# Performance work log

Hardware: AMD Instinct MI355X
Metric: run time of the kernel (lower is better)

The kernel has to match this reference:

```python
import jax, jax.numpy as jnp
import numpy as np
import math

B, N, DIM, H, DH, NNULL = 2, 2048, 1024, 16, 64, 2
SCALE = 8.0
LN_EPS = 1e-5


def _alibi_slopes(heads):
    # heads is a power of 2 here (16): slopes = start * start**i
    start = 2.0 ** (-(2.0 ** (-(math.log2(heads) - 3))))
    return np.array([start * (start ** i) for i in range(heads)], dtype=np.float32)


def setup_inputs() -> dict:
    key = jax.random.key(0)
    ks = jax.random.split(key, 6)
    inner = H * DH
    return {
        "x": jax.random.normal(ks[0], (B, N, DIM), dtype=jnp.float32),
        "norm_g": jnp.ones((DIM,), jnp.float32),
        "norm_b": jnp.zeros((DIM,), jnp.float32),
        "Wq": jax.random.normal(ks[1], (DIM, inner), jnp.float32) * 0.02,
        "Wkv": jax.random.normal(ks[2], (DIM, 2 * inner), jnp.float32) * 0.02,
        "q_scale": jnp.ones((DH,), jnp.float32),
        "k_scale": jnp.ones((DH,), jnp.float32),
        "null_kv": jax.random.normal(ks[3], (H, 2 * NNULL, DH), jnp.float32),
        "Wout": jax.random.normal(ks[4], (inner, DIM), jnp.float32) * 0.02,
    }


def _l2norm(t):
    # matches F.normalize: x / max(||x||, 1e-12)
    n = jnp.sqrt(jnp.sum(t * t, axis=-1, keepdims=True))
    return t / jnp.maximum(n, 1e-12)


def reference(x, norm_g, norm_b, Wq, Wkv, q_scale, k_scale, null_kv, Wout):
    b, n, dim = x.shape
    h, dh, nn = H, DH, NNULL
    j = n + nn

    # NOTE: faithful to source -- K/V come from the PRE-norm x (kv_input bound
    # before x = self.norm(x)); only Q uses the LayerNorm'd x.
    mu = jnp.mean(x, axis=-1, keepdims=True)
    var = jnp.mean((x - mu) ** 2, axis=-1, keepdims=True)
    xn = (x - mu) * jax.lax.rsqrt(var + LN_EPS) * norm_g + norm_b

    q = (xn @ Wq).reshape(b, n, h, dh).transpose(0, 2, 1, 3)          # b h n d
    kv = x @ Wkv
    k, v = jnp.split(kv, 2, axis=-1)
    k = k.reshape(b, n, h, dh).transpose(0, 2, 1, 3)                   # b h n d
    v = v.reshape(b, n, h, dh).transpose(0, 2, 1, 3)

    # null kv: (h, 2*nn, dh) -> (h, nn, 2, dh)
    null = null_kv.reshape(h, nn, 2, dh)
    nk = jnp.broadcast_to(null[:, :, 0, :][None], (b, h, nn, dh))
    nv = jnp.broadcast_to(null[:, :, 1, :][None], (b, h, nn, dh))
    k = jnp.concatenate([nk, k], axis=2)                               # b h j d
    v = jnp.concatenate([nv, v], axis=2)

    q = _l2norm(q) * q_scale
    k = _l2norm(k) * k_scale

    sim = jnp.einsum('bhid,bhjd->bhij', q, k) * SCALE                  # b h n j

    # ALiBi bias: rows at positions j-n..j-1, cols 0..j-1
    irow = jnp.arange(j - n, j)
    jcol = jnp.arange(j)
    bias = -jnp.abs(jcol[None, :] - irow[:, None]).astype(sim.dtype)   # (n, j)
    slopes = jnp.asarray(_alibi_slopes(h))[:, None, None]              # (h,1,1)
    sim = sim + slopes * bias

    # causal mask: triu with offset j - n + 1 (null kv always visible)
    causal = jnp.triu(jnp.ones((n, j), dtype=bool), k=j - n + 1)
    neg = jnp.finfo(sim.dtype).max
    sim = jnp.where(causal[None, None], -neg, sim)

    attn = jax.nn.softmax(sim, axis=-1)
    out = jnp.einsum('bhij,bhjd->bhid', attn, v)
    out = out.transpose(0, 2, 1, 3).reshape(b, n, h * dh)
    return out @ Wout
```

## Files before the change

kernel.cpp:

```cpp
#include <hip/hip_runtime.h>
#include <hip/hip_bf16.h>
#include <stdint.h>

#define H_    16
#define N_    2048
#define DIM_  1024
#define DH_   64
#define NN_   2
#define J_    2050
#define JP_   2112
#define B_    2
#define M_    4096
#define NSEG_ 84

typedef unsigned short u16;
typedef unsigned int u32;
typedef short bf16x8 __attribute__((ext_vector_type(8)));
typedef float f32x4 __attribute__((ext_vector_type(4)));

__device__ __forceinline__ u16 f2b(float f) {
  union { float f; unsigned int i; } v; v.f = f;
  unsigned int r = v.i + 0x7fffu + ((v.i >> 16) & 1u);
  return (u16)(r >> 16);
}
__device__ __forceinline__ float b2f(u16 u) {
  union { unsigned int i; float f; } v; v.i = ((unsigned int)u) << 16; return v.f;
}
__device__ __forceinline__ float lo2f(u32 u) {
  union { u32 i; float f; } v; v.i = u << 16; return v.f;
}
__device__ __forceinline__ float hi2f(u32 u) {
  union { u32 i; float f; } v; v.i = u & 0xffff0000u; return v.f;
}
__device__ __forceinline__ void unp8(const uint4 u, float* d) {
  d[0] = lo2f(u.x); d[1] = hi2f(u.x); d[2] = lo2f(u.y); d[3] = hi2f(u.y);
  d[4] = lo2f(u.z); d[5] = hi2f(u.z); d[6] = lo2f(u.w); d[7] = hi2f(u.w);
}
__device__ __forceinline__ u32 pk2(float a, float b) {
  union { __hip_bfloat162 h; u32 u; } x;
  x.h = __float22bfloat162_rn(make_float2(a, b));
  return x.u;
}
__device__ __forceinline__ void dma16(const u16* g, u16* l) {
  __builtin_amdgcn_global_load_lds(
      (const __attribute__((address_space(1))) u32*)(const void*)g,
      (__attribute__((address_space(3))) u32*)(void*)l, 16, 0, 0);
}

__global__ __launch_bounds__(256) void ktranspose_cast(const float* __restrict__ in,
                                                       u16* __restrict__ out, int R, int C) {
  __shared__ float tile[32][33];
  int tx = threadIdx.x & 31, ty = threadIdx.x >> 5;
  int c0 = blockIdx.x * 32, r0 = blockIdx.y * 32;
  #pragma unroll
  for (int i = 0; i < 32; i += 8)
    tile[ty + i][tx] = in[(size_t)(r0 + ty + i) * C + c0 + tx];
  __syncthreads();
  #pragma unroll
  for (int i = 0; i < 32; i += 8)
    out[(size_t)(c0 + ty + i) * R + r0 + tx] = f2b(tile[tx][ty + i]);
}

__global__ __launch_bounds__(256) void lnorm_k(const float* __restrict__ x,
                                               const float* __restrict__ g,
                                               const float* __restrict__ bb,
                                               u16* __restrict__ xn,
                                               u16* __restrict__ xbf) {
  int row = blockIdx.x;
  int t = threadIdx.x;
  float4 rw = *(const float4*)(x + (size_t)row * DIM_ + t * 4);
  float v0 = rw.x, v1 = rw.y, v2 = rw.z, v3 = rw.w;
  uint2 cw;
  cw.x = pk2(v0, v1);
  cw.y = pk2(v2, v3);
  *(uint2*)(xbf + (size_t)row * DIM_ + t * 4) = cw;
  float s = v0 + v1 + v2 + v3;
  float ss = v0 * v0 + v1 * v1 + v2 * v2 + v3 * v3;
  #pragma unroll
  for (int o = 32; o; o >>= 1) { s += __shfl_xor(s, o, 64); ss += __shfl_xor(ss, o, 64); }
  __shared__ float red[8];
  int lane = t & 63, w = t >> 6;
  if (lane == 0) { red[w] = s; red[4 + w] = ss; }
  __syncthreads();
  float S = red[0] + red[1] + red[2] + red[3];
  float SS = red[4] + red[5] + red[6] + red[7];
  float mu = S * (1.0f / DIM_);
  float var = SS * (1.0f / DIM_) - mu * mu;
  float rs = rsqrtf(var + 1e-5f);
  float4 gv = *(const float4*)(g + t * 4);
  float4 bv = *(const float4*)(bb + t * 4);
  uint2 ow;
  ow.x = pk2((v0 - mu) * rs * gv.x + bv.x, (v1 - mu) * rs * gv.y + bv.y);
  ow.y = pk2((v2 - mu) * rs * gv.z + bv.z, (v3 - mu) * rs * gv.w + bv.w);
  *(uint2*)(xn + (size_t)row * DIM_ + t * 4) = ow;
}

template <int MODE>
__global__ __launch_bounds__(256) void gemm_k(const u16* __restrict__ A,
                                              const u16* __restrict__ BT,
                                              void* __restrict__ dst0,
                                              void* __restrict__ dst1,
                                              const float* __restrict__ scale,
                                              int M, int Nc, int K) {
  __shared__ u16 As[128 * 64];
  __shared__ u16 Bs[64 * 64];
  int tid = threadIdx.x, wv = tid >> 6, lane = tid & 63;
  int fm = lane & 15, fg = lane >> 4;
  int row0 = blockIdx.y * 128, col0 = blockIdx.x * 64;
  f32x4 acc[2][4] = {};
  int srow = lane >> 3;
  int skb = ((lane & 7) ^ srow) * 8;
  const u16* Ag = A + (size_t)(row0 + wv * 32 + srow) * K + skb;
  const u16* Bg = BT + (size_t)(col0 + wv * 16 + srow) * K + skb;
  u16* AsW = As + (wv * 32) * 64;
  u16* BsW = Bs + (wv * 16) * 64;
  int fr7 = fm & 7;
  int ak0 = (fg ^ fr7) * 8;
  int ak1 = ((fg + 4) ^ fr7) * 8;
  for (int k0 = 0; k0 < K; k0 += 64) {
    __syncthreads();
    dma16(Ag + k0,                    AsW);
    dma16(Ag + (size_t)8 * K + k0,    AsW + 8 * 64);
    dma16(Ag + (size_t)16 * K + k0,   AsW + 16 * 64);
    dma16(Ag + (size_t)24 * K + k0,   AsW + 24 * 64);
    dma16(Bg + k0,                    BsW);
    dma16(Bg + (size_t)8 * K + k0,    BsW + 8 * 64);
    __syncthreads();
    bf16x8 af0[2], af1[2], bf0[4], bf1[4];
    #pragma unroll
    for (int mt = 0; mt < 2; mt++) {
      int rbase = (wv * 32 + mt * 16 + fm) * 64;
      af0[mt] = *(const bf16x8*)&As[rbase + ak0];
      af1[mt] = *(const bf16x8*)&As[rbase + ak1];
    }
    #pragma unroll
    for (int nt = 0; nt < 4; nt++) {
      int rbase = (nt * 16 + fm) * 64;
      bf0[nt] = *(const bf16x8*)&Bs[rbase + ak0];
      bf1[nt] = *(const bf16x8*)&Bs[rbase + ak1];
    }
    #pragma unroll
    for (int mt = 0; mt < 2; mt++)
      #pragma unroll
      for (int nt = 0; nt < 4; nt++) {
        acc[mt][nt] = __builtin_amdgcn_mfma_f32_16x16x32_bf16(af0[mt], bf0[nt], acc[mt][nt], 0, 0, 0);
        acc[mt][nt] = __builtin_amdgcn_mfma_f32_16x16x32_bf16(af1[mt], bf1[nt], acc[mt][nt], 0, 0, 0);
      }
  }
  if (MODE == 1) {
    float* C = (float*)dst0;
    #pragma unroll
    for (int mt = 0; mt < 2; mt++)
      #pragma unroll
      for (int r = 0; r < 4; r++) {
        int m = row0 + wv * 32 + mt * 16 + fg * 4 + r;
        #pragma unroll
        for (int nt = 0; nt < 4; nt++)
          C[(size_t)m * Nc + col0 + nt * 16 + fm] = acc[mt][nt][r];
      }
  } else {
    bool isK = (MODE == 2) || (col0 < 1024);
    int h = (isK ? col0 : col0 - 1024) >> 6;
    float sv[4];
    if (isK) {
      #pragma unroll
      for (int nt = 0; nt < 4; nt++) sv[nt] = scale[nt * 16 + fm];
    }
    u16* Do = (u16*)((MODE == 3 && !isK) ? dst1 : dst0);
    #pragma unroll
    for (int mt = 0; mt < 2; mt++) {
      #pragma unroll
      for (int r = 0; r < 4; r++) {
        float inv = 1.0f;
        if (isK) {
          float ssp = 0.0f;
          #pragma unroll
          for (int nt = 0; nt < 4; nt++) ssp += acc[mt][nt][r] * acc[mt][nt][r];
          #pragma unroll
          for (int o = 1; o <= 8; o <<= 1) ssp += __shfl_xor(ssp, o, 64);
          inv = 1.0f / fmaxf(sqrtf(ssp), 1e-12f);
        }
        int m = row0 + wv * 32 + mt * 16 + fg * 4 + r;
        int b = m >> 11, n = m & 2047;
        size_t base;
        if (MODE == 2)      base = (((size_t)(b * H_ + h)) * N_ + n) * 64;
        else if (isK)       base = (((size_t)(b * H_ + h)) * JP_ + (n + NN_)) * 64;
        else                base = (((size_t)(b * H_ + h)) * J_ + (n + NN_)) * 64;
        #pragma unroll
        for (int nt = 0; nt < 4; nt++) {
          float val = acc[mt][nt][r];
          if (isK) val = val * inv * sv[nt];
          Do[base + nt * 16 + fm] = f2b(val);
        }
      }
    }
  }
}

__global__ __launch_bounds__(256) void vtransp_k(const u16* __restrict__ Vb,
                                                 const float* __restrict__ nkv,
                                                 const float* __restrict__ ks,
                                                 u16* __restrict__ Kb,
                                                 u16* __restrict__ VTp) {
  __shared__ u16 tile[64][80];
  int t = threadIdx.x;
  int c = blockIdx.x, bh = blockIdx.y, h = bh & 15;
  int jl = t >> 2, dc = (t & 3) * 16;
  int j = c * 64 + jl;
  if (j < NN_) {
    float kvv[16];
    float kssp = 0.0f;
    #pragma unroll
    for (int e = 0; e < 16; e++) {
      float vv = nkv[(size_t)(h * 4 + 2 * j + 1) * 64 + dc + e];
      tile[jl][dc + e] = f2b(vv);
      float kv = nkv[(size_t)(h * 4 + 2 * j) * 64 + dc + e];
      kvv[e] = kv; kssp += kv * kv;
    }
    kssp += __shfl_xor(kssp, 1, 64);
    kssp += __shfl_xor(kssp, 2, 64);
    float inv = 1.0f / fmaxf(sqrtf(kssp), 1e-12f);
    #pragma unroll
    for (int e = 0; e < 16; e++)
      Kb[((size_t)bh * JP_ + j) * 64 + dc + e] = f2b(kvv[e] * inv * ks[dc + e]);
  } else if (j < J_) {
    const uint4* src = (const uint4*)(Vb + ((size_t)bh * J_ + j) * 64 + dc);
    *(uint4*)&tile[jl][dc] = src[0];
    *(uint4*)&tile[jl][dc + 8] = src[1];
  } else {
    uint4 z = {0, 0, 0, 0};
    *(uint4*)&tile[jl][dc] = z;
    *(uint4*)&tile[jl][dc + 8] = z;
  }
  __syncthreads();
  int d = t >> 2, p0 = (t & 3) * 16;
  u16 tmp[16] __attribute__((aligned(16)));
  #pragma unroll
  for (int e = 0; e < 16; e++) {
    int pos = p0 + e;
    int h2 = pos >> 5, rem = pos & 31;
    int fgp = rem >> 3, tt = rem & 7;
    int nt = tt >> 2, r = tt & 3;
    int jloc = (h2 * 2 + nt) * 16 + fgp * 4 + r;
    tmp[e] = tile[jloc][d];
  }
  uint4* dstp = (uint4*)(VTp + ((size_t)bh * 64 + d) * JP_ + c * 64 + p0);
  dstp[0] = ((uint4*)tmp)[0];
  dstp[1] = ((uint4*)tmp)[1];
}

__global__ __launch_bounds__(256, 6) void attn_k(const u16* __restrict__ Qn,
                                                 const u16* __restrict__ Kb,
                                                 const u16* __restrict__ VTp,
                                                 const float* __restrict__ qs,
                                                 const float* __restrict__ ks,
                                                 u16* __restrict__ partials) {
  __shared__ u16 Ks0[64 * 32], Ks1[64 * 32];
  __shared__ u16 Vs0[64 * 32], Vs1[64 * 32];
  int tid = threadIdx.x;
  int wv = tid >> 6, lane = tid & 63;
  int fm = lane & 15, fg = lane >> 4;
  int bh = blockIdx.y, h = bh & 15;
  int cum = 0, qt = 0, seg = 0;
  #pragma unroll 1
  for (int i = 0; i < 32; i++) {
    int t = 31 - i, s = (t + 9) >> 3;
    if ((int)blockIdx.x < cum + s) { qt = t; seg = (int)blockIdx.x - cum; break; }
    cum += s;
  }
  int q0 = qt * 64;
  int q = q0 + wv * 16 + fm;
  float slope = exp2f(-0.5f * (float)(h + 1));
  float prod = fabsf(qs[lane] * ks[lane]);
  #pragma unroll
  for (int o = 32; o; o >>= 1) prod = fmaxf(prod, __shfl_xor(prod, o, 64));
  float Mb = 8.0f * prod;
  const u16* qp = Qn + ((size_t)bh * N_ + q) * 64 + fg * 8;
  bf16x8 qf0 = *(const bf16x8*)(qp);
  bf16x8 qf1 = *(const bf16x8*)(qp + 32);
  f32x4 accO[4] = {};
  float lp = 0.0f;
  int lr = lane >> 2;
  int kbs = ((lane & 3) ^ ((lane >> 3) & 3)) * 8;
  int fs = (fg ^ ((fm >> 1) & 3)) * 8;
  const u16* KbBH = Kb + (size_t)bh * JP_ * 64;
  const u16* VTbh = VTp + (size_t)bh * 64 * JP_;
  int c0 = seg * 8;
  int c1 = min(c0 + 8, qt + 2);
  for (int c = c0; c < c1; c++) {
    int jb = c * 64;
    __syncthreads();
    const u16* Kg = KbBH + (size_t)(jb + wv * 16 + lr) * 64 + kbs;
    dma16(Kg,      Ks0 + wv * 512);
    dma16(Kg + 32, Ks1 + wv * 512);
    const u16* Vg = VTbh + (size_t)(wv * 16 + lr) * JP_ + jb + kbs;
    dma16(Vg,      Vs0 + wv * 512);
    dma16(Vg + 32, Vs1 + wv * 512);
    __syncthreads();
    f32x4 accS[4] = {};
    #pragma unroll
    for (int nt = 0; nt < 4; nt++) {
      bf16x8 kf0 = *(const bf16x8*)&Ks0[(nt * 16 + fm) * 32 + fs];
      accS[nt] = __builtin_amdgcn_mfma_f32_16x16x32_bf16(kf0, qf0, accS[nt], 0, 0, 0);
      bf16x8 kf1 = *(const bf16x8*)&Ks1[(nt * 16 + fm) * 32 + fs];
      accS[nt] = __builtin_amdgcn_mfma_f32_16x16x32_bf16(kf1, qf1, accS[nt], 0, 0, 0);
    }
    union { bf16x8 v; u16 s[8]; } P0, P1;
    #pragma unroll
    for (int nt = 0; nt < 4; nt++) {
      #pragma unroll
      for (int r = 0; r < 4; r++) {
        int jj = jb + nt * 16 + fg * 4 + r;
        float arg = fmaf(accS[nt][r], 8.0f, slope * (float)(jj - q - 2)) - Mb;
        float p = (jj <= q + 2) ? __expf(arg) : 0.0f;
        u16 pb = f2b(p);
        lp += b2f(pb);
        if (nt < 2) P0.s[nt * 4 + r] = pb;
        else        P1.s[(nt - 2) * 4 + r] = pb;
      }
    }
    #pragma unroll
    for (int nt = 0; nt < 4; nt++) {
      bf16x8 vf0 = *(const bf16x8*)&Vs0[(nt * 16 + fm) * 32 + fs];
      accO[nt] = __builtin_amdgcn_mfma_f32_16x16x32_bf16(vf0, P0.v, accO[nt], 0, 0, 0);
      bf16x8 vf1 = *(const bf16x8*)&Vs1[(nt * 16 + fm) * 32 + fs];
      accO[nt] = __builtin_amdgcn_mfma_f32_16x16x32_bf16(vf1, P1.v, accO[nt], 0, 0, 0);
    }
  }
  lp += __shfl_xor(lp, 16, 64);
  lp += __shfl_xor(lp, 32, 64);
  u16* P = partials + ((size_t)bh * NSEG_ + blockIdx.x) * 4224;
  int sq = wv * 16 + fm;
  #pragma unroll
  for (int nt = 0; nt < 4; nt++) {
    uint2 ow;
    ow.x = pk2(accO[nt][0], accO[nt][1]);
    ow.y = pk2(accO[nt][2], accO[nt][3]);
    *(uint2*)(P + sq * 64 + nt * 16 + fg * 4) = ow;
  }
  if (fg == 0) *(float*)(P + 4096 + 2 * sq) = lp;
}

__global__ __launch_bounds__(256) void comb_k(const u16* __restrict__ partials,
                                              u16* __restrict__ AO) {
  int qt = blockIdx.x, bh = blockIdx.y, b = bh >> 4, h = bh & 15;
  int t = threadIdx.x, q = t >> 2, dq = (t & 3) * 16;
  int s = (qt + 9) >> 3;
  int cum = 0;
  for (int tt = qt + 1; tt < 32; tt++) cum += (tt + 9) >> 3;
  float acc[16] = {};
  float lsum = 0.0f;
  for (int k = 0; k < s; k++) {
    const u16* P = partials + ((size_t)bh * NSEG_ + cum + k) * 4224;
    uint4 a = *(const uint4*)(P + q * 64 + dq);
    uint4 bq = *(const uint4*)(P + q * 64 + dq + 8);
    float tmp[8];
    unp8(a, tmp);
    #pragma unroll
    for (int e = 0; e < 8; e++) acc[e] += tmp[e];
    unp8(bq, tmp);
    #pragma unroll
    for (int e = 0; e < 8; e++) acc[8 + e] += tmp[e];
    lsum += *(const float*)(P + 4096 + 2 * q);
  }
  float linv = 1.0f / lsum;
  int n = qt * 64 + q;
  u16* dst = AO + (((size_t)(b * N_ + n)) * H_ + h) * 64 + dq;
  u16 ov[16] __attribute__((aligned(16)));
  #pragma unroll
  for (int e = 0; e < 16; e++) ov[e] = f2b(acc[e] * linv);
  *(uint4*)dst = ((uint4*)ov)[0];
  *(uint4*)(dst + 8) = ((uint4*)ov)[1];
}

extern "C" void kernel_launch(void* const* d_in, const int* in_sizes, int n_in,
                              void* d_out, int out_size, void* d_ws, size_t ws_size,
                              hipStream_t stream) {
  const float* x    = (const float*)d_in[0];
  const float* ng   = (const float*)d_in[1];
  const float* nb   = (const float*)d_in[2];
  const float* Wq   = (const float*)d_in[3];
  const float* Wkv  = (const float*)d_in[4];
  const float* qs   = (const float*)d_in[5];
  const float* ks   = (const float*)d_in[6];
  const float* nkv  = (const float*)d_in[7];
  const float* Wout = (const float*)d_in[8];
  float* out = (float*)d_out;
  char* ws = (char*)d_ws;

  u16* xn    = (u16*)(ws + 0);
  u16* WoutT = (u16*)(ws + 8388608);
  u16* Qn    = (u16*)(ws + 10485760);
  u16* Kb    = (u16*)(ws + 18874368);
  u16* VTp   = (u16*)(ws + 27525120);
  u16* xbf   = (u16*)(ws + 36175872);
  u16* WqT   = (u16*)(ws + 44564480);
  u16* WkvT  = (u16*)(ws + 46661632);
  u16* Vb    = (u16*)(ws + 50855936);
  u16* parts = xbf;
  u16* AO    = xn;

  hipMemsetAsync(Kb, 0, 8650752, stream);
  ktranspose_cast<<<dim3(32, 32), 256, 0, stream>>>(Wq, WqT, 1024, 1024);
  ktranspose_cast<<<dim3(64, 32), 256, 0, stream>>>(Wkv, WkvT, 1024, 2048);
  ktranspose_cast<<<dim3(32, 32), 256, 0, stream>>>(Wout, WoutT, 1024, 1024);
  lnorm_k<<<4096, 256, 0, stream>>>(x, ng, nb, xn, xbf);
  gemm_k<2><<<dim3(16, 32), 256, 0, stream>>>(xn, WqT, Qn, nullptr, qs, M_, 1024, 1024);
  gemm_k<3><<<dim3(32, 32), 256, 0, stream>>>(xbf, WkvT, Kb, Vb, ks, M_, 2048, 1024);
  vtransp_k<<<dim3(33, 32), 256, 0, stream>>>(Vb, nkv, ks, Kb, VTp);
  attn_k<<<dim3(NSEG_, 32), 256, 0, stream>>>(Qn, Kb, VTp, qs, ks, parts);
  comb_k<<<dim3(32, 32), 256, 0, stream>>>(parts, AO);
  gemm_k<1><<<dim3(16, 32), 256, 0, stream>>>(AO, WoutT, out, nullptr, nullptr, M_, 1024, 1024);
}
```

Before: 231.3 us.

## Merge launches and load GEMM A-operand directly into registers with prefetch

Merges the three weight transposes into one launch and the Q and KV projections into one GEMM launch, which cuts launch count and tail effects. The full-buffer memset of K is dropped; only the padding rows are zeroed inside the V-transpose kernel. The GEMM core now loads A fragments straight from global memory into registers, prefetched one K-step ahead, instead of staging them in LDS. This removes LDS traffic and part of the sync cost, but A reads are no longer shared through LDS across waves, and each lane issues strided global loads.

```diff
diff --git a/kernel.cpp b/kernel.cpp
--- a/kernel.cpp
+++ b/kernel.cpp
@@ -47,11 +47,21 @@
       (__attribute__((address_space(3))) u32*)(void*)l, 16, 0, 0);
 }
 
-__global__ __launch_bounds__(256) void ktranspose_cast(const float* __restrict__ in,
-                                                       u16* __restrict__ out, int R, int C) {
+__global__ __launch_bounds__(256) void wtrans_k(const float* __restrict__ Wq,
+                                                const float* __restrict__ Wkv,
+                                                const float* __restrict__ Wout,
+                                                u16* __restrict__ WqT,
+                                                u16* __restrict__ WkvT,
+                                                u16* __restrict__ WoutT) {
   __shared__ float tile[32][33];
+  int bx = blockIdx.x;
+  const float* in; u16* out; int C, cx;
+  if (bx < 32)      { in = Wq;   out = WqT;   C = 1024; cx = bx; }
+  else if (bx < 96) { in = Wkv;  out = WkvT;  C = 2048; cx = bx - 32; }
+  else              { in = Wout; out = WoutT; C = 1024; cx = bx - 96; }
+  const int R = 1024;
   int tx = threadIdx.x & 31, ty = threadIdx.x >> 5;
-  int c0 = blockIdx.x * 32, r0 = blockIdx.y * 32;
+  int c0 = cx * 32, r0 = blockIdx.y * 32;
   #pragma unroll
   for (int i = 0; i < 32; i += 8)
     tile[ty + i][tx] = in[(size_t)(r0 + ty + i) * C + c0 + tx];
@@ -95,106 +105,131 @@
   *(uint2*)(xn + (size_t)row * DIM_ + t * 4) = ow;
 }
 
-template <int MODE>
-__global__ __launch_bounds__(256) void gemm_k(const u16* __restrict__ A,
-                                              const u16* __restrict__ BT,
-                                              void* __restrict__ dst0,
-                                              void* __restrict__ dst1,
-                                              const float* __restrict__ scale,
-                                              int M, int Nc, int K) {
-  __shared__ u16 As[128 * 64];
+__device__ __forceinline__ void gemm_core(const u16* __restrict__ A,
+                                          const u16* __restrict__ BT,
+                                          int row0, int col0, int wv, int lane,
+                                          u16* __restrict__ Bs, f32x4 acc[2][4]) {
+  int fm = lane & 15, fg = lane >> 4;
+  int srow = lane >> 3;
+  int skb = ((lane & 7) ^ srow) * 8;
+  const u16* Bg = BT + (size_t)(col0 + wv * 16 + srow) * 1024 + skb;
+  u16* BsW = Bs + (wv * 16) * 64;
+  const u16* Ag = A + (size_t)(row0 + wv * 32 + fm) * 1024 + fg * 8;
+  int fr7 = fm & 7;
+  int ak0 = (fg ^ fr7) * 8;
+  int ak1 = ((fg + 4) ^ fr7) * 8;
+  bf16x8 a0[2], a1[2];
+  a0[0] = *(const bf16x8*)(Ag);
+  a0[1] = *(const bf16x8*)(Ag + 16 * 1024);
+  a1[0] = *(const bf16x8*)(Ag + 32);
+  a1[1] = *(const bf16x8*)(Ag + 16 * 1024 + 32);
+  for (int k0 = 0; k0 < 1024; k0 += 64) {
+    __syncthreads();
+    dma16(Bg + k0,                   BsW);
+    dma16(Bg + (size_t)8 * 1024 + k0, BsW + 8 * 64);
+    __syncthreads();
+    bf16x8 b0[4], b1[4];
+    #pragma unroll
+    for (int nt = 0; nt < 4; nt++) {
+      int rbase = (nt * 16 + fm) * 64;
+      b0[nt] = *(const bf16x8*)&Bs[rbase + ak0];
+      b1[nt] = *(const bf16x8*)&Bs[rbase + ak1];
+    }
+    int kn = (k0 + 64 < 1024) ? k0 + 64 : 960;
+    bf16x8 na0[2], na1[2];
+    {
+      const u16* An = Ag + kn;
+      na0[0] = *(const bf16x8*)(An);
+      na0[1] = *(const bf16x8*)(An + 16 * 1024);
+      na1[0] = *(const bf16x8*)(An + 32);
+      na1[1] = *(const bf16x8*)(An + 16 * 1024 + 32);
+    }
+    #pragma unroll
+    for (int mt = 0; mt < 2; mt++)
+      #pragma unroll
+      for (int nt = 0; nt < 4; nt++) {
+        acc[mt][nt] = __builtin_amdgcn_mfma_f32_16x16x32_bf16(a0[mt], b0[nt], acc[mt][nt], 0, 0, 0);
+        acc[mt][nt] = __builtin_amdgcn_mfma_f32_16x16x32_bf16(a1[mt], b1[nt], acc[mt][nt], 0, 0, 0);
+      }
+    a0[0] = na0[0]; a0[1] = na0[1]; a1[0] = na1[0]; a1[1] = na1[1];
+  }
+}
+
+__global__ __launch_bounds__(256) void gemm_qkv(const u16* __restrict__ xn,
+                                                const u16* __restrict__ xbf,
+                                                const u16* __restrict__ WqT,
+                                                const u16* __restrict__ WkvT,
+                                                u16* __restrict__ Qn,
+                                                u16* __restrict__ Kb,
+                                                u16* __restrict__ Vb,
+                                                const float* __restrict__ qs,
+                                                const float* __restrict__ ks) {
+  __shared__ u16 Bs[64 * 64];
+  int tid = threadIdx.x, wv = tid >> 6, lane = tid & 63;
+  int fm = lane & 15, fg = lane >> 4;
+  int bx = blockIdx.x, row0 = blockIdx.y * 128;
+  bool qpath = bx < 16;
+  const u16* A  = qpath ? xn : xbf;
+  const u16* BT = qpath ? WqT : WkvT;
+  int col0 = qpath ? bx * 64 : (bx - 16) * 64;
+  f32x4 acc[2][4] = {};
+  gemm_core(A, BT, row0, col0, wv, lane, Bs, acc);
+  bool isK = qpath || (col0 < 1024);
+  int h = (qpath ? col0 : (isK ? col0 : col0 - 1024)) >> 6;
+  const float* sc = qpath ? qs : ks;
+  float sv[4];
+  if (isK) {
+    #pragma unroll
+    for (int nt = 0; nt < 4; nt++) sv[nt] = sc[nt * 16 + fm];
+  }
+  u16* Do = qpath ? Qn : (isK ? Kb : Vb);
+  #pragma unroll
+  for (int mt = 0; mt < 2; mt++) {
+    #pragma unroll
+    for (int r = 0; r < 4; r++) {
+      float inv = 1.0f;
+      if (isK) {
+        float ssp = 0.0f;
+        #pragma unroll
+        for (int nt = 0; nt < 4; nt++) ssp += acc[mt][nt][r] * acc[mt][nt][r];
+        #pragma unroll
+        for (int o = 1; o <= 8; o <<= 1) ssp += __shfl_xor(ssp, o, 64);
+        inv = 1.0f / fmaxf(sqrtf(ssp), 1e-12f);
+      }
+      int m = row0 + wv * 32 + mt * 16 + fg * 4 + r;
+      int b = m >> 11, n = m & 2047;
+      size_t base;
+      if (qpath)     base = (((size_t)(b * H_ + h)) * N_ + n) * 64;
+      else if (isK)  base = (((size_t)(b * H_ + h)) * JP_ + (n + NN_)) * 64;
+      else           base = (((size_t)(b * H_ + h)) * J_ + (n + NN_)) * 64;
+      #pragma unroll
+      for (int nt = 0; nt < 4; nt++) {
+        float val = acc[mt][nt][r];
+        if (isK) val = val * inv * sv[nt];
+        Do[base + nt * 16 + fm] = f2b(val);
+      }
+    }
+  }
+}
+
+__global__ __launch_bounds__(256) void gemm_out(const u16* __restrict__ AO,
+                                                const u16* __restrict__ WoutT,
+                                                float* __restrict__ out) {
   __shared__ u16 Bs[64 * 64];
   int tid = threadIdx.x, wv = tid >> 6, lane = tid & 63;
   int fm = lane & 15, fg = lane >> 4;
   int row0 = blockIdx.y * 128, col0 = blockIdx.x * 64;
   f32x4 acc[2][4] = {};
-  int srow = lane >> 3;
-  int skb = ((lane & 7) ^ srow) * 8;
-  const u16* Ag = A + (size_t)(row0 + wv * 32 + srow) * K + skb;
-  const u16* Bg = BT + (size_t)(col0 + wv * 16 + srow) * K + skb;
-  u16* AsW = As + (wv * 32) * 64;
-  u16* BsW = Bs + (wv * 16) * 64;
-  int fr7 = fm & 7;
-  int ak0 = (fg ^ fr7) * 8;
-  int ak1 = ((fg + 4) ^ fr7) * 8;
-  for (int k0 = 0; k0 < K; k0 += 64) {
-    __syncthreads();
-    dma16(Ag + k0,                    AsW);
-    dma16(Ag + (size_t)8 * K + k0,    AsW + 8 * 64);
-    dma16(Ag + (size_t)16 * K + k0,   AsW + 16 * 64);
-    dma16(Ag + (size_t)24 * K + k0,   AsW + 24 * 64);
-    dma16(Bg + k0,                    BsW);
-    dma16(Bg + (size_t)8 * K + k0,    BsW + 8 * 64);
-    __syncthreads();
-    bf16x8 af0[2], af1[2], bf0[4], bf1[4];
-    #pragma unroll
-    for (int mt = 0; mt < 2; mt++) {
-      int rbase = (wv * 32 + mt * 16 + fm) * 64;
-      af0[mt] = *(const bf16x8*)&As[rbase + ak0];
-      af1[mt] = *(const bf16x8*)&As[rbase + ak1];
-    }
-    #pragma unroll
-    for (int nt = 0; nt < 4; nt++) {
-      int rbase = (nt * 16 + fm) * 64;
-      bf0[nt] = *(const bf16x8*)&Bs[rbase + ak0];
-      bf1[nt] = *(const bf16x8*)&Bs[rbase + ak1];
-    }
-    #pragma unroll
-    for (int mt = 0; mt < 2; mt++)
+  gemm_core(AO, WoutT, row0, col0, wv, lane, Bs, acc);
+  #pragma unroll
+  for (int mt = 0; mt < 2; mt++)
+    #pragma unroll
+    for (int r = 0; r < 4; r++) {
+      int m = row0 + wv * 32 + mt * 16 + fg * 4 + r;
       #pragma unroll
-      for (int nt = 0; nt < 4; nt++) {
-        acc[mt][nt] = __builtin_amdgcn_mfma_f32_16x16x32_bf16(af0[mt], bf0[nt], acc[mt][nt], 0, 0, 0);
-        acc[mt][nt] = __builtin_amdgcn_mfma_f32_16x16x32_bf16(af1[mt], bf1[nt], acc[mt][nt], 0, 0, 0);
-      }
-  }
-  if (MODE == 1) {
-    float* C = (float*)dst0;
-    #pragma unroll
-    for (int mt = 0; mt < 2; mt++)
-      #pragma unroll
-      for (int r = 0; r < 4; r++) {
-        int m = row0 + wv * 32 + mt * 16 + fg * 4 + r;
-        #pragma unroll
-        for (int nt = 0; nt < 4; nt++)
-          C[(size_t)m * Nc + col0 + nt * 16 + fm] = acc[mt][nt][r];
-      }
-  } else {
-    bool isK = (MODE == 2) || (col0 < 1024);
-    int h = (isK ? col0 : col0 - 1024) >> 6;
-    float sv[4];
-    if (isK) {
-      #pragma unroll
-      for (int nt = 0; nt < 4; nt++) sv[nt] = scale[nt * 16 + fm];
-    }
-    u16* Do = (u16*)((MODE == 3 && !isK) ? dst1 : dst0);
-    #pragma unroll
-    for (int mt = 0; mt < 2; mt++) {
-      #pragma unroll
-      for (int r = 0; r < 4; r++) {
-        float inv = 1.0f;
-        if (isK) {
-          float ssp = 0.0f;
-          #pragma unroll
-          for (int nt = 0; nt < 4; nt++) ssp += acc[mt][nt][r] * acc[mt][nt][r];
-          #pragma unroll
-          for (int o = 1; o <= 8; o <<= 1) ssp += __shfl_xor(ssp, o, 64);
-          inv = 1.0f / fmaxf(sqrtf(ssp), 1e-12f);
-        }
-        int m = row0 + wv * 32 + mt * 16 + fg * 4 + r;
-        int b = m >> 11, n = m & 2047;
-        size_t base;
-        if (MODE == 2)      base = (((size_t)(b * H_ + h)) * N_ + n) * 64;
-        else if (isK)       base = (((size_t)(b * H_ + h)) * JP_ + (n + NN_)) * 64;
-        else                base = (((size_t)(b * H_ + h)) * J_ + (n + NN_)) * 64;
-        #pragma unroll
-        for (int nt = 0; nt < 4; nt++) {
-          float val = acc[mt][nt][r];
-          if (isK) val = val * inv * sv[nt];
-          Do[base + nt * 16 + fm] = f2b(val);
-        }
-      }
-    }
-  }
+      for (int nt = 0; nt < 4; nt++)
+        out[(size_t)m * 1024 + col0 + nt * 16 + fm] = acc[mt][nt][r];
+    }
 }
 
 __global__ __launch_bounds__(256) void vtransp_k(const u16* __restrict__ Vb,
@@ -231,6 +266,8 @@
     uint4 z = {0, 0, 0, 0};
     *(uint4*)&tile[jl][dc] = z;
     *(uint4*)&tile[jl][dc + 8] = z;
+    uint4* kz = (uint4*)(Kb + ((size_t)bh * JP_ + j) * 64 + dc);
+    kz[0] = z; kz[1] = z;
   }
   __syncthreads();
   int d = t >> 2, p0 = (t & 3) * 16;
@@ -400,15 +437,11 @@
   u16* parts = xbf;
   u16* AO    = xn;
 
-  hipMemsetAsync(Kb, 0, 8650752, stream);
-  ktranspose_cast<<<dim3(32, 32), 256, 0, stream>>>(Wq, WqT, 1024, 1024);
-  ktranspose_cast<<<dim3(64, 32), 256, 0, stream>>>(Wkv, WkvT, 1024, 2048);
-  ktranspose_cast<<<dim3(32, 32), 256, 0, stream>>>(Wout, WoutT, 1024, 1024);
+  wtrans_k<<<dim3(128, 32), 256, 0, stream>>>(Wq, Wkv, Wout, WqT, WkvT, WoutT);
   lnorm_k<<<4096, 256, 0, stream>>>(x, ng, nb, xn, xbf);
-  gemm_k<2><<<dim3(16, 32), 256, 0, stream>>>(xn, WqT, Qn, nullptr, qs, M_, 1024, 1024);
-  gemm_k<3><<<dim3(32, 32), 256, 0, stream>>>(xbf, WkvT, Kb, Vb, ks, M_, 2048, 1024);
+  gemm_qkv<<<dim3(48, 32), 256, 0, stream>>>(xn, xbf, WqT, WkvT, Qn, Kb, Vb, qs, ks);
   vtransp_k<<<dim3(33, 32), 256, 0, stream>>>(Vb, nkv, ks, Kb, VTp);
   attn_k<<<dim3(NSEG_, 32), 256, 0, stream>>>(Qn, Kb, VTp, qs, ks, parts);
   comb_k<<<dim3(32, 32), 256, 0, stream>>>(parts, AO);
-  gemm_k<1><<<dim3(16, 32), 256, 0, stream>>>(AO, WoutT, out, nullptr, nullptr, M_, 1024, 1024);
-}
+  gemm_out<<<dim3(16, 32), 256, 0, stream>>>(AO, WoutT, out);
+}
```

Result: slower. 240.9 us (+4.2%).
